# Kernel tuning notes

Measured on AMD Instinct MI355X. Metric: run time of the kernel, lower is better.

The kernel has to match this reference:

```python
import jax, jax.numpy as jnp
import numpy as np

N_NODES = 100000
N_FULL = 1000000
N_EDGES = 500000
D_FEAT = 128


def setup_inputs() -> dict:
    key = jax.random.key(0)
    k1, k2, k3, k4, k5, k6 = jax.random.split(key, 6)
    h = jax.random.normal(k1, (N_NODES, D_FEAT), dtype=jnp.float32)
    # popularity counts >= 1 so ipw = 1/pop is well-behaved
    pop = jax.random.uniform(k2, (N_NODES, 1), dtype=jnp.float32) + 1.0
    bias = jax.random.normal(k3, (N_FULL,), dtype=jnp.float32)
    src = jax.random.randint(k4, (N_EDGES,), 0, N_NODES, dtype=jnp.int64)
    dst = jax.random.randint(k5, (N_EDGES,), 0, N_NODES, dtype=jnp.int64)
    nid = jax.random.randint(k6, (N_NODES,), 0, N_FULL, dtype=jnp.int64)
    return {"h": h, "pop": pop, "bias": bias, "src": src, "dst": dst, "nid": nid}


def reference(h, pop, bias, src, dst, nid):
    # u_dot_v('h','h','s'): per-edge dot product of endpoint features -> [E]
    s = jnp.sum(h[src] * h[dst], axis=-1)
    # ipw = 1/pop per node ([N,1]); u_dot_v('ipw','ipw') -> product of scalars per edge
    ipw = 1.0 / pop  # [N, 1]
    ipw_score = jnp.sum(ipw[src] * ipw[dst], axis=-1)  # [E]
    # bias gather-add: bias indexed by full-graph node ids of edge endpoints
    s = s + bias[nid[src]] + bias[nid[dst]]
    pair_score = s * ipw_score
    return pair_score
```

## Files before the change

### kernel.cpp

```cpp
#include <hip/hip_runtime.h>
#include <hip/hip_fp16.h>


union H8 {
    float4  f4;
    __half2 h2[4];
};

__device__ inline float dot8(const H8& a, const H8& b) {
    float s = 0.0f;
#pragma unroll
    for (int k = 0; k < 4; ++k) {
        float2 fa = __half22float2(a.h2[k]);
        float2 fb = __half22float2(b.h2[k]);
        s += fa.x * fb.x + fa.y * fb.y;
    }
    return s;
}

__global__ __launch_bounds__(256) void convert_h_kernel(
    const float* __restrict__ h,
    __half*      __restrict__ h16,
    int n_elems)
{
    int i = blockIdx.x * blockDim.x + threadIdx.x;
    int base = i * 8;
    if (base < n_elems) {
        const float4 f0 = *reinterpret_cast<const float4*>(h + base);
        const float4 f1 = *reinterpret_cast<const float4*>(h + base + 4);
        H8 o;
        o.h2[0] = __floats2half2_rn(f0.x, f0.y);
        o.h2[1] = __floats2half2_rn(f0.z, f0.w);
        o.h2[2] = __floats2half2_rn(f1.x, f1.y);
        o.h2[3] = __floats2half2_rn(f1.z, f1.w);
        *reinterpret_cast<float4*>(h16 + base) = o.f4;
    }
}

__global__ __launch_bounds__(256) void node_prep_kernel(
    const float* __restrict__ pop,
    const float* __restrict__ bias,
    const int*   __restrict__ nid,
    float2*      __restrict__ nodeinfo,
    int n_nodes)
{
    int i = blockIdx.x * blockDim.x + threadIdx.x;
    if (i < n_nodes) {
        nodeinfo[i] = make_float2(1.0f / pop[i], bias[nid[i]]);
    }
}

__global__ __launch_bounds__(256) void edge_score_f16_kernel(
    const __half* __restrict__ h16,
    const float2* __restrict__ nodeinfo,
    const int*    __restrict__ src,
    const int*    __restrict__ dst,
    float*        __restrict__ out,
    int n_edges)
{
    const int gtid = blockIdx.x * blockDim.x + threadIdx.x;
    const int e    = gtid >> 3;
    const int lane = threadIdx.x & 7;
    if (e >= n_edges) return;

    const int si = src[e];
    const int di = dst[e];

    const __half* ra = h16 + (size_t)si * 128 + lane * 16;
    const __half* rb = h16 + (size_t)di * 128 + lane * 16;

    H8 a0, a1, b0, b1;
    a0.f4 = *reinterpret_cast<const float4*>(ra);
    a1.f4 = *reinterpret_cast<const float4*>(ra + 8);
    b0.f4 = *reinterpret_cast<const float4*>(rb);
    b1.f4 = *reinterpret_cast<const float4*>(rb + 8);

    float part = dot8(a0, b0) + dot8(a1, b1);

    part += __shfl_xor(part, 1);
    part += __shfl_xor(part, 2);
    part += __shfl_xor(part, 4);

    if (lane == 0) {
        const float2 ns = nodeinfo[si];
        const float2 nd = nodeinfo[di];
        out[e] = (part + ns.y + nd.y) * (ns.x * nd.x);
    }
}


__global__ __launch_bounds__(256) void edge_score_f32_kernel(
    const float*  __restrict__ h,
    const float2* __restrict__ nodeinfo,
    const int*    __restrict__ src,
    const int*    __restrict__ dst,
    float*        __restrict__ out,
    int n_edges)
{
    const int gtid = blockIdx.x * blockDim.x + threadIdx.x;
    const int e    = gtid >> 4;
    const int lane = threadIdx.x & 15;
    if (e >= n_edges) return;

    const int si = src[e];
    const int di = dst[e];
    const float* ra = h + (size_t)si * 128 + lane * 8;
    const float* rb = h + (size_t)di * 128 + lane * 8;
    const float4 a0 = *reinterpret_cast<const float4*>(ra);
    const float4 a1 = *reinterpret_cast<const float4*>(ra + 4);
    const float4 b0 = *reinterpret_cast<const float4*>(rb);
    const float4 b1 = *reinterpret_cast<const float4*>(rb + 4);

    float part = a0.x * b0.x + a0.y * b0.y + a0.z * b0.z + a0.w * b0.w
               + a1.x * b1.x + a1.y * b1.y + a1.z * b1.z + a1.w * b1.w;

    part += __shfl_xor(part, 1);
    part += __shfl_xor(part, 2);
    part += __shfl_xor(part, 4);
    part += __shfl_xor(part, 8);

    if (lane == 0) {
        const float2 ns = nodeinfo[si];
        const float2 nd = nodeinfo[di];
        out[e] = (part + ns.y + nd.y) * (ns.x * nd.x);
    }
}

__global__ __launch_bounds__(256) void edge_score_fallback_kernel(
    const float* __restrict__ h,
    const float* __restrict__ pop,
    const float* __restrict__ bias,
    const int*   __restrict__ src,
    const int*   __restrict__ dst,
    const int*   __restrict__ nid,
    float*       __restrict__ out,
    int n_edges)
{
    const int gtid = blockIdx.x * blockDim.x + threadIdx.x;
    const int e    = gtid >> 4;
    const int lane = threadIdx.x & 15;
    if (e >= n_edges) return;

    const int si = src[e];
    const int di = dst[e];
    const float* ra = h + (size_t)si * 128 + lane * 8;
    const float* rb = h + (size_t)di * 128 + lane * 8;
    const float4 a0 = *reinterpret_cast<const float4*>(ra);
    const float4 a1 = *reinterpret_cast<const float4*>(ra + 4);
    const float4 b0 = *reinterpret_cast<const float4*>(rb);
    const float4 b1 = *reinterpret_cast<const float4*>(rb + 4);

    float part = a0.x * b0.x + a0.y * b0.y + a0.z * b0.z + a0.w * b0.w
               + a1.x * b1.x + a1.y * b1.y + a1.z * b1.z + a1.w * b1.w;

    part += __shfl_xor(part, 1);
    part += __shfl_xor(part, 2);
    part += __shfl_xor(part, 4);
    part += __shfl_xor(part, 8);

    if (lane == 0) {
        const float ipw = (1.0f / pop[si]) * (1.0f / pop[di]);
        const float bb  = bias[nid[si]] + bias[nid[di]];
        out[e] = (part + bb) * ipw;
    }
}

extern "C" void kernel_launch(void* const* d_in, const int* in_sizes, int n_in,
                              void* d_out, int out_size, void* d_ws, size_t ws_size,
                              hipStream_t stream) {
    const float* h    = (const float*)d_in[0];
    const float* pop  = (const float*)d_in[1];
    const float* bias = (const float*)d_in[2];
    const int*   src  = (const int*)d_in[3];
    const int*   dst  = (const int*)d_in[4];
    const int*   nid  = (const int*)d_in[5];
    float*       out  = (float*)d_out;

    const int n_edges = in_sizes[3];
    const int n_nodes = in_sizes[1];
    const int n_elems = in_sizes[0];

    const size_t h16_bytes  = (size_t)n_elems * sizeof(__half);
    const size_t info_bytes = (size_t)n_nodes * sizeof(float2);

    if (ws_size >= h16_bytes + info_bytes) {
        __half* h16      = (__half*)d_ws;
        float2* nodeinfo = (float2*)((char*)d_ws + h16_bytes);

        int cgrid = (n_elems / 8 + 255) / 256;
        convert_h_kernel<<<cgrid, 256, 0, stream>>>(h, h16, n_elems);

        int pgrid = (n_nodes + 255) / 256;
        node_prep_kernel<<<pgrid, 256, 0, stream>>>(pop, bias, nid, nodeinfo, n_nodes);

        int grid = ((n_edges * 8) + 255) / 256;
        edge_score_f16_kernel<<<grid, 256, 0, stream>>>(h16, nodeinfo, src, dst,
                                                        out, n_edges);
    } else if (ws_size >= info_bytes) {
        float2* nodeinfo = (float2*)d_ws;

        int pgrid = (n_nodes + 255) / 256;
        node_prep_kernel<<<pgrid, 256, 0, stream>>>(pop, bias, nid, nodeinfo, n_nodes);

        int grid = ((n_edges * 16) + 255) / 256;
        edge_score_f32_kernel<<<grid, 256, 0, stream>>>(h, nodeinfo, src, dst,
                                                        out, n_edges);
    } else {
        int grid = ((n_edges * 16) + 255) / 256;
        edge_score_fallback_kernel<<<grid, 256, 0, stream>>>(h, pop, bias, src, dst, nid,
                                                             out, n_edges);
    }
}
```

Measured before the change: 55.66 us.

## Bucket-sort edges by source node before scoring to improve gather locality

Result: slower. 120.1 us (+115.7%).

```diff
diff --git a/kernel.cpp b/kernel.cpp
--- a/kernel.cpp
+++ b/kernel.cpp
@@ -1,6 +1,8 @@
 #include <hip/hip_runtime.h>
 #include <hip/hip_fp16.h>
 
+
+#define BUCKET_SHIFT 3
 
 union H8 {
     float4  f4;
@@ -50,6 +52,108 @@
     }
 }
 
+__global__ __launch_bounds__(256) void zero_kernel(
+    unsigned* __restrict__ p, int n)
+{
+    int i = blockIdx.x * blockDim.x + threadIdx.x;
+    if (i < n) p[i] = 0u;
+}
+
+__global__ __launch_bounds__(256) void hist_kernel(
+    const int* __restrict__ src,
+    unsigned*  __restrict__ counts,
+    int n_edges)
+{
+    int e = blockIdx.x * blockDim.x + threadIdx.x;
+    if (e < n_edges) {
+        atomicAdd(&counts[src[e] >> BUCKET_SHIFT], 1u);
+    }
+}
+
+__global__ __launch_bounds__(1024) void scan_kernel(
+    const unsigned* __restrict__ counts,
+    unsigned*       __restrict__ cursors,
+    int nb)
+{
+    __shared__ unsigned partial[1024];
+    const int tid   = threadIdx.x;
+    const int chunk = (nb + 1023) / 1024;
+    const int lo    = tid * chunk;
+    const int hi    = min(lo + chunk, nb);
+
+    unsigned s = 0;
+    for (int i = lo; i < hi; ++i) s += counts[i];
+    partial[tid] = s;
+    __syncthreads();
+
+    for (int off = 1; off < 1024; off <<= 1) {
+        unsigned v = (tid >= off) ? partial[tid - off] : 0u;
+        __syncthreads();
+        partial[tid] += v;
+        __syncthreads();
+    }
+
+    unsigned base = (tid == 0) ? 0u : partial[tid - 1];
+    for (int i = lo; i < hi; ++i) {
+        cursors[i] = base;
+        base += counts[i];
+    }
+}
+
+__global__ __launch_bounds__(256) void scatter_kernel(
+    const int* __restrict__ src,
+    const int* __restrict__ dst,
+    unsigned*  __restrict__ cursors,
+    int4*      __restrict__ rec,
+    int n_edges)
+{
+    int e = blockIdx.x * blockDim.x + threadIdx.x;
+    if (e < n_edges) {
+        const int si = src[e];
+        const unsigned pos = atomicAdd(&cursors[si >> BUCKET_SHIFT], 1u);
+        rec[pos] = make_int4(si, dst[e], e, 0);
+    }
+}
+
+__global__ __launch_bounds__(256) void edge_score_sorted_kernel(
+    const __half* __restrict__ h16,
+    const float2* __restrict__ nodeinfo,
+    const int4*   __restrict__ rec,
+    float*        __restrict__ out,
+    int n_edges)
+{
+    const int gtid = blockIdx.x * blockDim.x + threadIdx.x;
+    const int k    = gtid >> 3;
+    const int lane = threadIdx.x & 7;
+    if (k >= n_edges) return;
+
+    const int4 r  = rec[k];
+    const int  si = r.x;
+    const int  di = r.y;
+
+    const __half* ra = h16 + (size_t)si * 128 + lane * 8;
+    const __half* rb = h16 + (size_t)di * 128 + lane * 8;
+
+    H8 a0, a1, b0, b1;
+    a0.f4 = *reinterpret_cast<const float4*>(ra);
+    a1.f4 = *reinterpret_cast<const float4*>(ra + 64);
+    b0.f4 = *reinterpret_cast<const float4*>(rb);
+    b1.f4 = *reinterpret_cast<const float4*>(rb + 64);
+
+    float part = dot8(a0, b0) + dot8(a1, b1);
+
+    part += __shfl_xor(part, 1);
+    part += __shfl_xor(part, 2);
+    part += __shfl_xor(part, 4);
+
+    if (lane == 0) {
+        const float2 ns = nodeinfo[si];
+        const float2 nd = nodeinfo[di];
+        out[r.z] = (part + ns.y + nd.y) * (ns.x * nd.x);
+    }
+}
+
+
 __global__ __launch_bounds__(256) void edge_score_f16_kernel(
     const __half* __restrict__ h16,
     const float2* __restrict__ nodeinfo,
@@ -65,59 +169,20 @@
 
     const int si = src[e];
     const int di = dst[e];
-
-    const __half* ra = h16 + (size_t)si * 128 + lane * 16;
-    const __half* rb = h16 + (size_t)di * 128 + lane * 16;
+    const __half* ra = h16 + (size_t)si * 128 + lane * 8;
+    const __half* rb = h16 + (size_t)di * 128 + lane * 8;
 
     H8 a0, a1, b0, b1;
     a0.f4 = *reinterpret_cast<const float4*>(ra);
-    a1.f4 = *reinterpret_cast<const float4*>(ra + 8);
+    a1.f4 = *reinterpret_cast<const float4*>(ra + 64);
     b0.f4 = *reinterpret_cast<const float4*>(rb);
-    b1.f4 = *reinterpret_cast<const float4*>(rb + 8);
+    b1.f4 = *reinterpret_cast<const float4*>(rb + 64);
 
     float part = dot8(a0, b0) + dot8(a1, b1);
 
     part += __shfl_xor(part, 1);
     part += __shfl_xor(part, 2);
     part += __shfl_xor(part, 4);
-
-    if (lane == 0) {
-        const float2 ns = nodeinfo[si];
-        const float2 nd = nodeinfo[di];
-        out[e] = (part + ns.y + nd.y) * (ns.x * nd.x);
-    }
-}
-
-
-__global__ __launch_bounds__(256) void edge_score_f32_kernel(
-    const float*  __restrict__ h,
-    const float2* __restrict__ nodeinfo,
-    const int*    __restrict__ src,
-    const int*    __restrict__ dst,
-    float*        __restrict__ out,
-    int n_edges)
-{
-    const int gtid = blockIdx.x * blockDim.x + threadIdx.x;
-    const int e    = gtid >> 4;
-    const int lane = threadIdx.x & 15;
-    if (e >= n_edges) return;
-
-    const int si = src[e];
-    const int di = dst[e];
-    const float* ra = h + (size_t)si * 128 + lane * 8;
-    const float* rb = h + (size_t)di * 128 + lane * 8;
-    const float4 a0 = *reinterpret_cast<const float4*>(ra);
-    const float4 a1 = *reinterpret_cast<const float4*>(ra + 4);
-    const float4 b0 = *reinterpret_cast<const float4*>(rb);
-    const float4 b1 = *reinterpret_cast<const float4*>(rb + 4);
-
-    float part = a0.x * b0.x + a0.y * b0.y + a0.z * b0.z + a0.w * b0.w
-               + a1.x * b1.x + a1.y * b1.y + a1.z * b1.z + a1.w * b1.w;
-
-    part += __shfl_xor(part, 1);
-    part += __shfl_xor(part, 2);
-    part += __shfl_xor(part, 4);
-    part += __shfl_xor(part, 8);
 
     if (lane == 0) {
         const float2 ns = nodeinfo[si];
@@ -179,11 +244,43 @@
     const int n_edges = in_sizes[3];
     const int n_nodes = in_sizes[1];
     const int n_elems = in_sizes[0];
-
-    const size_t h16_bytes  = (size_t)n_elems * sizeof(__half);
-    const size_t info_bytes = (size_t)n_nodes * sizeof(float2);
-
-    if (ws_size >= h16_bytes + info_bytes) {
+    const int n_buckets = (n_nodes + (1 << BUCKET_SHIFT) - 1) >> BUCKET_SHIFT;
+
+    auto align256 = [](size_t x) { return (x + 255) & ~(size_t)255; };
+
+    const size_t h16_bytes  = align256((size_t)n_elems * sizeof(__half));
+    const size_t info_bytes = align256((size_t)n_nodes * sizeof(float2));
+    const size_t cnt_bytes  = align256((size_t)n_buckets * sizeof(unsigned));
+    const size_t rec_bytes  = align256((size_t)n_edges * sizeof(int4));
+    const size_t full_bytes = h16_bytes + info_bytes + 2 * cnt_bytes + rec_bytes;
+
+    if (ws_size >= full_bytes) {
+        char* p = (char*)d_ws;
+        __half*   h16      = (__half*)p;              p += h16_bytes;
+        float2*   nodeinfo = (float2*)p;              p += info_bytes;
+        unsigned* counts   = (unsigned*)p;            p += cnt_bytes;
+        unsigned* cursors  = (unsigned*)p;            p += cnt_bytes;
+        int4*     rec      = (int4*)p;
+
+        int cgrid = (n_elems / 8 + 255) / 256;
+        convert_h_kernel<<<cgrid, 256, 0, stream>>>(h, h16, n_elems);
+
+        int pgrid = (n_nodes + 255) / 256;
+        node_prep_kernel<<<pgrid, 256, 0, stream>>>(pop, bias, nid, nodeinfo, n_nodes);
+
+        zero_kernel<<<(n_buckets + 255) / 256, 256, 0, stream>>>(counts, n_buckets);
+
+        int egrid = (n_edges + 255) / 256;
+        hist_kernel<<<egrid, 256, 0, stream>>>(src, counts, n_edges);
+
+        scan_kernel<<<1, 1024, 0, stream>>>(counts, cursors, n_buckets);
+
+        scatter_kernel<<<egrid, 256, 0, stream>>>(src, dst, cursors, rec, n_edges);
+
+        int grid = ((n_edges * 8) + 255) / 256;
+        edge_score_sorted_kernel<<<grid, 256, 0, stream>>>(h16, nodeinfo, rec,
+                                                           out, n_edges);
+    } else if (ws_size >= h16_bytes + info_bytes) {
         __half* h16      = (__half*)d_ws;
         float2* nodeinfo = (float2*)((char*)d_ws + h16_bytes);
 
@@ -195,15 +292,6 @@
 
         int grid = ((n_edges * 8) + 255) / 256;
         edge_score_f16_kernel<<<grid, 256, 0, stream>>>(h16, nodeinfo, src, dst,
-                                                        out, n_edges);
-    } else if (ws_size >= info_bytes) {
-        float2* nodeinfo = (float2*)d_ws;
-
-        int pgrid = (n_nodes + 255) / 256;
-        node_prep_kernel<<<pgrid, 256, 0, stream>>>(pop, bias, nid, nodeinfo, n_nodes);
-
-        int grid = ((n_edges * 16) + 255) / 256;
-        edge_score_f32_kernel<<<grid, 256, 0, stream>>>(h, nodeinfo, src, dst,
                                                         out, n_edges);
     } else {
         int grid = ((n_edges * 16) + 255) / 256;
```
